# Performance work log

Measured on AMD Instinct MI355X. Metric: run time of the kernel, lower is better.

Reference implementation:

```python
import jax, jax.numpy as jnp
import numpy as np
import math

K = 8
MOMENTUM = 0.999


def _gelu(x):
    c = math.sqrt(2.0 / math.pi)
    return 0.5 * x * (1.0 + jnp.tanh(c * (x + 0.044715 * x ** 3)))


def _normalize(v, eps=1e-12):
    n = jnp.linalg.norm(v, axis=-1, keepdims=True)
    return v / jnp.maximum(n, eps)


def setup_inputs() -> dict:
    key = jax.random.key(0)
    k1, k2 = jax.random.split(key)
    B, T, D = 4, 4096, 2048
    x = jax.random.normal(k1, (B, T, D), dtype=jnp.float32)
    prototypes = _normalize(jax.random.normal(k2, (K, D), dtype=jnp.float32))
    log_tau = jnp.asarray(math.log(2.0), dtype=jnp.float32)
    log_blend = jnp.asarray(math.log(0.3 / 0.7), dtype=jnp.float32)
    return {"x": x, "prototypes": prototypes, "log_tau": log_tau, "log_blend": log_blend}


def reference(x, prototypes, log_tau, log_blend):
    tau = jnp.exp(log_tau)
    alpha = jax.nn.sigmoid(log_blend)
    B, T, D = x.shape
    x_flat = jax.lax.stop_gradient(x.reshape(-1, D))  # [N, D], detached

    P_norm = _normalize(prototypes)                  # [K, D]
    xn = _normalize(x_flat, eps=1e-8)                # [N, D]

    sims = jnp.clip(xn @ P_norm.T, -1.0, 1.0)        # [N, K]
    assignments = jnp.argmax(sims, axis=-1)          # [N]

    # masked per-cluster mean via segment-sum (vectorized over K)
    sums = jax.ops.segment_sum(x_flat, assignments, num_segments=K)       # [K, D]
    counts = jax.ops.segment_sum(jnp.ones((x_flat.shape[0],), x.dtype),
                                 assignments, num_segments=K)             # [K]
    has = (counts > 0)[:, None]
    centroids = jnp.where(has, sums / jnp.maximum(counts, 1.0)[:, None], prototypes)
    new_P = _normalize(centroids)

    P2 = MOMENTUM * prototypes + (1.0 - MOMENTUM) * new_P
    P2n = _normalize(P2, eps=1e-8)

    sims2 = jnp.clip(xn @ P2n.T, -1.0, 1.0)          # [N, K]
    dists = jnp.clip(1.0 - jnp.max(sims2, axis=-1), 0.0, 2.0)
    novelty = (1.0 - jnp.exp(-tau * dists)).reshape(B, T)

    scale = jnp.clip(1.0 - alpha + alpha * novelty[..., None], 0.1, 10.0)
    return _gelu(x * scale)
```

## Files before the change

kernel.cpp:

```cpp
#include <hip/hip_runtime.h>

#define N_TOK 16384
#define DDIM  2048
#define KC    8
#define CH1   32
#define TBA   4
#define TBF   4

typedef float nfloat4 __attribute__((ext_vector_type(4)));

__device__ __forceinline__ void nt_store4(const float4& v, float* p){
  nfloat4 nv; nv.x = v.x; nv.y = v.y; nv.z = v.z; nv.w = v.w;
  __builtin_nontemporal_store(nv, (nfloat4*)p);
}
__device__ __forceinline__ float4 nt_load4(const float* p){
  nfloat4 nv = __builtin_nontemporal_load((const nfloat4*)p);
  return make_float4(nv.x, nv.y, nv.z, nv.w);
}

__device__ __forceinline__ float wave_sum(float v){
  #pragma unroll
  for (int off = 32; off > 0; off >>= 1)
    v += __shfl_xor(v, off, 64);
  return v;
}

__device__ __forceinline__ float butterfly8(float v[8], int t){
  {
    const bool h = (t & 1);
    #pragma unroll
    for (int j = 0; j < 4; ++j){
      float s    = h ? v[j]   : v[j+4];
      float keep = h ? v[j+4] : v[j];
      v[j] = keep + __shfl_xor(s, 1, 64);
    }
  }
  {
    const bool h = (t & 2);
    #pragma unroll
    for (int j = 0; j < 2; ++j){
      float s    = h ? v[j]   : v[j+2];
      float keep = h ? v[j+2] : v[j];
      v[j] = keep + __shfl_xor(s, 2, 64);
    }
  }
  {
    const bool h = (t & 4);
    float s    = h ? v[0] : v[1];
    float keep = h ? v[1] : v[0];
    v[0] = keep + __shfl_xor(s, 4, 64);
  }
  v[0] += __shfl_xor(v[0], 8, 64);
  v[0] += __shfl_xor(v[0], 16, 64);
  v[0] += __shfl_xor(v[0], 32, 64);
  return v[0];
}

__device__ __forceinline__ float gelu_tanh(float v){
  const float c = 0.7978845608028654f;
  float tt = c * v * (1.0f + 0.044715f * v * v);
  float e  = __expf(2.0f * tt);
  float th = 1.0f - 2.0f / (e + 1.0f);
  return 0.5f * v * (1.0f + th);
}

__global__ __launch_bounds__(256, 2)
void k_assign(const float* __restrict__ x, const float* __restrict__ proto,
              float* __restrict__ psums, float* __restrict__ pcnts, int ntok)
{
  const int t = threadIdx.x;
  const int wave = t >> 6, lane = t & 63;
  const int d0 = 4*t, d1 = DDIM/2 + 4*t;
  const int kidx = ((lane&1)<<2) | (lane&2) | ((lane>>2)&1);

  __shared__ float rednorm[4*KC];
  __shared__ float red[TBA][4][KC];
  __shared__ float sInv[KC];
  __shared__ float sCnt[KC];
  __shared__ int   sAsg[TBA];

  float4 P0[KC], P1[KC];
  float4 acc0[KC], acc1[KC];
  #pragma unroll
  for (int k = 0; k < KC; ++k){
    P0[k] = *(const float4*)(proto + k*DDIM + d0);
    P1[k] = *(const float4*)(proto + k*DDIM + d1);
    acc0[k] = make_float4(0.f,0.f,0.f,0.f);
    acc1[k] = make_float4(0.f,0.f,0.f,0.f);
  }
  if (t < KC) sCnt[t] = 0.f;

  #pragma unroll
  for (int k = 0; k < KC; ++k){
    float ss = P0[k].x*P0[k].x + P0[k].y*P0[k].y + P0[k].z*P0[k].z + P0[k].w*P0[k].w
             + P1[k].x*P1[k].x + P1[k].y*P1[k].y + P1[k].z*P1[k].z + P1[k].w*P1[k].w;
    ss = wave_sum(ss);
    if (lane == 0) rednorm[wave*KC + k] = ss;
  }
  __syncthreads();
  if (t < KC){
    float ss = rednorm[t] + rednorm[KC + t] + rednorm[2*KC + t] + rednorm[3*KC + t];
    sInv[t] = 1.0f / fmaxf(sqrtf(ss), 1e-12f);
  }
  __syncthreads();

  const int stride = gridDim.x * TBA;
  float4 X0[TBA], X1[TBA], N0[TBA], N1[TBA];
  int tok0 = blockIdx.x * TBA;
  #pragma unroll
  for (int i = 0; i < TBA; ++i){
    int tk = tok0 + i;
    X0[i] = make_float4(0,0,0,0); X1[i] = make_float4(0,0,0,0);
    if (tk < ntok){
      X0[i] = *(const float4*)(x + (size_t)tk*DDIM + d0);
      X1[i] = *(const float4*)(x + (size_t)tk*DDIM + d1);
    }
  }

  for (; tok0 < ntok; tok0 += stride){
    const int ntok0 = tok0 + stride;
    #pragma unroll
    for (int i = 0; i < TBA; ++i){
      int tk = ntok0 + i;
      N0[i] = make_float4(0,0,0,0); N1[i] = make_float4(0,0,0,0);
      if (tk < ntok){
        N0[i] = *(const float4*)(x + (size_t)tk*DDIM + d0);
        N1[i] = *(const float4*)(x + (size_t)tk*DDIM + d1);
      }
    }
    #pragma unroll
    for (int i = 0; i < TBA; ++i){
      float v[KC];
      #pragma unroll
      for (int k = 0; k < KC; ++k){
        v[k] = X0[i].x*P0[k].x + X0[i].y*P0[k].y + X0[i].z*P0[k].z + X0[i].w*P0[k].w
             + X1[i].x*P1[k].x + X1[i].y*P1[k].y + X1[i].z*P1[k].z + X1[i].w*P1[k].w;
      }
      float r = butterfly8(v, t);
      if (lane < 8) red[i][wave][kidx] = r;
    }
    __syncthreads();
    if (t < TBA && tok0 + t < ntok){
      int best = 0; float bv = -3.4e38f;
      #pragma unroll
      for (int k = 0; k < KC; ++k){
        float val = (red[t][0][k] + red[t][1][k] + red[t][2][k] + red[t][3][k]) * sInv[k];
        if (val > bv){ bv = val; best = k; }
      }
      sAsg[t] = best;
      atomicAdd(&sCnt[best], 1.0f);
    }
    __syncthreads();
    #pragma unroll
    for (int i = 0; i < TBA; ++i){
      if (tok0 + i < ntok){
        const int a = sAsg[i];
        #pragma unroll
        for (int k = 0; k < KC; ++k){
          if (a == k){
            acc0[k].x += X0[i].x; acc0[k].y += X0[i].y; acc0[k].z += X0[i].z; acc0[k].w += X0[i].w;
            acc1[k].x += X1[i].x; acc1[k].y += X1[i].y; acc1[k].z += X1[i].z; acc1[k].w += X1[i].w;
          }
        }
      }
    }
    #pragma unroll
    for (int i = 0; i < TBA; ++i){ X0[i] = N0[i]; X1[i] = N1[i]; }
  }
  __syncthreads();
  float* dst = psums + (size_t)blockIdx.x * (KC*DDIM);
  #pragma unroll
  for (int k = 0; k < KC; ++k){
    nt_store4(acc0[k], dst + k*DDIM + d0);
    nt_store4(acc1[k], dst + k*DDIM + d1);
  }
  if (t < KC) pcnts[blockIdx.x*KC + t] = sCnt[t];
}

__global__ __launch_bounds__(256)
void k_reduce1(const float* __restrict__ psums, const float* __restrict__ pcnts,
               float* __restrict__ stage2, float* __restrict__ cnt2, int nb, int cs)
{
  const int ch = blockIdx.x >> 4;
  const int g  = blockIdx.x & 15;
  const int col = g*1024 + threadIdx.x*4;
  const int b0 = ch*cs;

  float4 acc = make_float4(0.f,0.f,0.f,0.f);
  #pragma unroll 4
  for (int i = 0; i < cs; ++i){
    int b = b0 + i;
    if (b < nb){
      float4 v = nt_load4(psums + (size_t)b*(KC*DDIM) + col);
      acc.x += v.x; acc.y += v.y; acc.z += v.z; acc.w += v.w;
    }
  }
  *(float4*)(stage2 + (size_t)ch*(KC*DDIM) + col) = acc;

  if (g == 0 && threadIdx.x < KC){
    float c = 0.f;
    for (int i = 0; i < cs; ++i){
      int b = b0 + i;
      if (b < nb) c += pcnts[b*KC + threadIdx.x];
    }
    cnt2[ch*KC + threadIdx.x] = c;
  }
}

__global__ __launch_bounds__(256)
void k_reduce2(const float* __restrict__ stage2, const float* __restrict__ cnt2,
               const float* __restrict__ proto, float* __restrict__ centroid)
{
  __shared__ float cnt[KC];
  if (threadIdx.x < KC){
    float c = 0.f;
    #pragma unroll
    for (int ch = 0; ch < CH1; ++ch) c += cnt2[ch*KC + threadIdx.x];
    cnt[threadIdx.x] = c;
  }
  __syncthreads();
  const int col = blockIdx.x*1024 + threadIdx.x*4;
  float4 s = make_float4(0.f,0.f,0.f,0.f);
  #pragma unroll
  for (int ch = 0; ch < CH1; ++ch){
    float4 v = *(const float4*)(stage2 + (size_t)ch*(KC*DDIM) + col);
    s.x += v.x; s.y += v.y; s.z += v.z; s.w += v.w;
  }
  const int k = col >> 11;
  const float c = cnt[k];
  float4 o;
  if (c > 0.f){
    float inv = 1.0f / fmaxf(c, 1.f);
    o.x = s.x*inv; o.y = s.y*inv; o.z = s.z*inv; o.w = s.w*inv;
  } else {
    o = *(const float4*)(proto + col);
  }
  *(float4*)(centroid + col) = o;
}

__global__ void k_pupdate(const float* __restrict__ centroid, const float* __restrict__ proto,
                          float* __restrict__ p2n)
{
  const int t = threadIdx.x;
  const int w = t >> 6, lane = t & 63;
  float4 c[8], pr[8];
  float ss = 0.f;
  #pragma unroll
  for (int j = 0; j < 8; ++j){
    const int d = (j*64 + lane)*4;
    c[j]  = *(const float4*)(centroid + w*DDIM + d);
    pr[j] = *(const float4*)(proto    + w*DDIM + d);
    ss += c[j].x*c[j].x + c[j].y*c[j].y + c[j].z*c[j].z + c[j].w*c[j].w;
  }
  ss = wave_sum(ss);
  const float invc = 1.0f / fmaxf(sqrtf(ss), 1e-12f);
  const float m = 0.999f, om = 1.0f - 0.999f;
  float4 p2[8];
  float ss2 = 0.f;
  #pragma unroll
  for (int j = 0; j < 8; ++j){
    p2[j].x = m*pr[j].x + om*c[j].x*invc;
    p2[j].y = m*pr[j].y + om*c[j].y*invc;
    p2[j].z = m*pr[j].z + om*c[j].z*invc;
    p2[j].w = m*pr[j].w + om*c[j].w*invc;
    ss2 += p2[j].x*p2[j].x + p2[j].y*p2[j].y + p2[j].z*p2[j].z + p2[j].w*p2[j].w;
  }
  ss2 = wave_sum(ss2);
  const float inv2 = 1.0f / fmaxf(sqrtf(ss2), 1e-8f);
  #pragma unroll
  for (int j = 0; j < 8; ++j){
    const int d = (j*64 + lane)*4;
    float4 o;
    o.x = p2[j].x*inv2; o.y = p2[j].y*inv2; o.z = p2[j].z*inv2; o.w = p2[j].w*inv2;
    *(float4*)(p2n + w*DDIM + d) = o;
  }
}

__global__ __launch_bounds__(256, 2)
void k_final(const float* __restrict__ x, const float* __restrict__ p2n,
             const float* __restrict__ plog_tau, const float* __restrict__ plog_blend,
             float* __restrict__ out, int ntok)
{
  const int t = threadIdx.x;
  const int wave = t >> 6, lane = t & 63;
  const int d0 = 4*t, d1 = DDIM/2 + 4*t;
  const int kidx = ((lane&1)<<2) | (lane&2) | ((lane>>2)&1);

  __shared__ float red[TBF][4][KC];
  __shared__ float redss[TBF][4];
  __shared__ float sScale[TBF];

  float4 P0[KC], P1[KC];
  #pragma unroll
  for (int k = 0; k < KC; ++k){
    P0[k] = *(const float4*)(p2n + k*DDIM + d0);
    P1[k] = *(const float4*)(p2n + k*DDIM + d1);
  }
  const float tau   = __expf(plog_tau[0]);
  const float alpha = 1.0f / (1.0f + __expf(-plog_blend[0]));

  const int stride = gridDim.x * TBF;
  float4 X0[TBF], X1[TBF], N0[TBF], N1[TBF];
  int tok0 = blockIdx.x * TBF;
  #pragma unroll
  for (int i = 0; i < TBF; ++i){
    int tk = tok0 + i;
    X0[i] = make_float4(0,0,0,0); X1[i] = make_float4(0,0,0,0);
    if (tk < ntok){
      X0[i] = *(const float4*)(x + (size_t)tk*DDIM + d0);
      X1[i] = *(const float4*)(x + (size_t)tk*DDIM + d1);
    }
  }

  for (; tok0 < ntok; tok0 += stride){
    const int ntok0 = tok0 + stride;
    #pragma unroll
    for (int i = 0; i < TBF; ++i){
      int tk = ntok0 + i;
      N0[i] = make_float4(0,0,0,0); N1[i] = make_float4(0,0,0,0);
      if (tk < ntok){
        N0[i] = *(const float4*)(x + (size_t)tk*DDIM + d0);
        N1[i] = *(const float4*)(x + (size_t)tk*DDIM + d1);
      }
    }
    #pragma unroll
    for (int i = 0; i < TBF; ++i){
      float v[KC];
      #pragma unroll
      for (int k = 0; k < KC; ++k){
        v[k] = X0[i].x*P0[k].x + X0[i].y*P0[k].y + X0[i].z*P0[k].z + X0[i].w*P0[k].w
             + X1[i].x*P1[k].x + X1[i].y*P1[k].y + X1[i].z*P1[k].z + X1[i].w*P1[k].w;
      }
      float r = butterfly8(v, t);
      if (lane < 8) red[i][wave][kidx] = r;
      float ss = X0[i].x*X0[i].x + X0[i].y*X0[i].y + X0[i].z*X0[i].z + X0[i].w*X0[i].w
               + X1[i].x*X1[i].x + X1[i].y*X1[i].y + X1[i].z*X1[i].z + X1[i].w*X1[i].w;
      ss = wave_sum(ss);
      if (lane == 0) redss[i][wave] = ss;
    }
    __syncthreads();
    if (t < TBF && tok0 + t < ntok){
      float fss = redss[t][0] + redss[t][1] + redss[t][2] + redss[t][3];
      float inv = 1.0f / fmaxf(sqrtf(fss), 1e-8f);
      float mx = -3.4e38f;
      #pragma unroll
      for (int k = 0; k < KC; ++k){
        float val = red[t][0][k] + red[t][1][k] + red[t][2][k] + red[t][3][k];
        mx = fmaxf(mx, val);
      }
      float s    = fminf(fmaxf(mx * inv, -1.0f), 1.0f);
      float dist = fminf(fmaxf(1.0f - s, 0.0f), 2.0f);
      float nov  = 1.0f - __expf(-tau * dist);
      float sc   = 1.0f - alpha + alpha * nov;
      sScale[t]  = fminf(fmaxf(sc, 0.1f), 10.0f);
    }
    __syncthreads();
    #pragma unroll
    for (int i = 0; i < TBF; ++i){
      int tk = tok0 + i;
      if (tk < ntok){
        const float sc = sScale[i];
        float* o = out + (size_t)tk*DDIM;
        float4 o0, o1;
        o0.x = gelu_tanh(X0[i].x*sc); o0.y = gelu_tanh(X0[i].y*sc);
        o0.z = gelu_tanh(X0[i].z*sc); o0.w = gelu_tanh(X0[i].w*sc);
        o1.x = gelu_tanh(X1[i].x*sc); o1.y = gelu_tanh(X1[i].y*sc);
        o1.z = gelu_tanh(X1[i].z*sc); o1.w = gelu_tanh(X1[i].w*sc);
        nt_store4(o0, o + d0);
        nt_store4(o1, o + d1);
      }
    }
    #pragma unroll
    for (int i = 0; i < TBF; ++i){ X0[i] = N0[i]; X1[i] = N1[i]; }
  }
}

extern "C" void kernel_launch(void* const* d_in, const int* in_sizes, int n_in,
                              void* d_out, int out_size, void* d_ws, size_t ws_size,
                              hipStream_t stream)
{
  const float* x          = (const float*)d_in[0];
  const float* proto      = (const float*)d_in[1];
  const float* log_tau    = (const float*)d_in[2];
  const float* log_blend  = (const float*)d_in[3];
  float* out = (float*)d_out;
  float* ws  = (float*)d_ws;

  const int ntok = in_sizes[0] / DDIM;

  float* centroid = ws;
  float* p2n      = ws + 16384;
  float* pcnts    = ws + 32768;
  float* cnt2     = ws + 36864;
  float* stage2   = ws + 37120;
  float* psums    = ws + 37120 + CH1*KC*DDIM;

  long cap = (long)(ws_size / 4) - (37120 + CH1*KC*DDIM);
  int nb = (int)(cap / (KC * DDIM));
  if (nb > 512) nb = 512;
  if (nb < 1)  nb = 1;
  const int cs = (nb + CH1 - 1) / CH1;

  k_assign <<<nb,      256, 0, stream>>>(x, proto, psums, pcnts, ntok);
  k_reduce1<<<CH1*16,  256, 0, stream>>>(psums, pcnts, stage2, cnt2, nb, cs);
  k_reduce2<<<16,      256, 0, stream>>>(stage2, cnt2, proto, centroid);
  k_pupdate<<<1,       512, 0, stream>>>(centroid, proto, p2n);
  k_final  <<<512,     256, 0, stream>>>(x, p2n, log_tau, log_blend, out, ntok);
}
```

Baseline: 308.0 us.

## Fuse pipeline into one cooperative kernel with grid syncs and bf16 partial sums

```diff
diff --git a/kernel.cpp b/kernel.cpp
--- a/kernel.cpp
+++ b/kernel.cpp
@@ -1,21 +1,31 @@
 #include <hip/hip_runtime.h>
-
-#define N_TOK 16384
+#include <hip/hip_cooperative_groups.h>
+
+namespace cg = cooperative_groups;
+
 #define DDIM  2048
 #define KC    8
 #define CH1   32
 #define TBA   4
 #define TBF   4
+#define GRID  512
 
 typedef float nfloat4 __attribute__((ext_vector_type(4)));
+typedef unsigned short ushortv8 __attribute__((ext_vector_type(8)));
+typedef unsigned short ushortv4 __attribute__((ext_vector_type(4)));
 
 __device__ __forceinline__ void nt_store4(const float4& v, float* p){
   nfloat4 nv; nv.x = v.x; nv.y = v.y; nv.z = v.z; nv.w = v.w;
   __builtin_nontemporal_store(nv, (nfloat4*)p);
 }
-__device__ __forceinline__ float4 nt_load4(const float* p){
-  nfloat4 nv = __builtin_nontemporal_load((const nfloat4*)p);
-  return make_float4(nv.x, nv.y, nv.z, nv.w);
+
+__device__ __forceinline__ unsigned short f2bf(float f){
+  unsigned u = __float_as_uint(f);
+  u += 0x7fffu + ((u >> 16) & 1u);
+  return (unsigned short)(u >> 16);
+}
+__device__ __forceinline__ float bf2f(unsigned short h){
+  return __uint_as_float(((unsigned)h) << 16);
 }
 
 __device__ __forceinline__ float wave_sum(float v){
@@ -64,9 +74,9 @@
   return 0.5f * v * (1.0f + th);
 }
 
-__global__ __launch_bounds__(256, 2)
-void k_assign(const float* __restrict__ x, const float* __restrict__ proto,
-              float* __restrict__ psums, float* __restrict__ pcnts, int ntok)
+__device__ __forceinline__ void phase_assign(const float* __restrict__ x,
+    const float* __restrict__ proto, unsigned short* __restrict__ psums,
+    float* __restrict__ pcnts, int ntok, int bid, int gsz)
 {
   const int t = threadIdx.x;
   const int wave = t >> 6, lane = t & 63;
@@ -74,13 +84,12 @@
   const int kidx = ((lane&1)<<2) | (lane&2) | ((lane>>2)&1);
 
   __shared__ float rednorm[4*KC];
-  __shared__ float red[TBA][4][KC];
-  __shared__ float sInv[KC];
+  __shared__ float redA[TBA][4][KC];
+  __shared__ float sInvA[KC];
   __shared__ float sCnt[KC];
   __shared__ int   sAsg[TBA];
 
-  float4 P0[KC], P1[KC];
-  float4 acc0[KC], acc1[KC];
+  float4 P0[KC], P1[KC], acc0[KC], acc1[KC];
   #pragma unroll
   for (int k = 0; k < KC; ++k){
     P0[k] = *(const float4*)(proto + k*DDIM + d0);
@@ -100,13 +109,13 @@
   __syncthreads();
   if (t < KC){
     float ss = rednorm[t] + rednorm[KC + t] + rednorm[2*KC + t] + rednorm[3*KC + t];
-    sInv[t] = 1.0f / fmaxf(sqrtf(ss), 1e-12f);
+    sInvA[t] = 1.0f / fmaxf(sqrtf(ss), 1e-12f);
   }
   __syncthreads();
 
-  const int stride = gridDim.x * TBA;
+  const int stride = gsz * TBA;
   float4 X0[TBA], X1[TBA], N0[TBA], N1[TBA];
-  int tok0 = blockIdx.x * TBA;
+  int tok0 = bid * TBA;
   #pragma unroll
   for (int i = 0; i < TBA; ++i){
     int tk = tok0 + i;
@@ -137,14 +146,14 @@
              + X1[i].x*P1[k].x + X1[i].y*P1[k].y + X1[i].z*P1[k].z + X1[i].w*P1[k].w;
       }
       float r = butterfly8(v, t);
-      if (lane < 8) red[i][wave][kidx] = r;
+      if (lane < 8) redA[i][wave][kidx] = r;
     }
     __syncthreads();
     if (t < TBA && tok0 + t < ntok){
       int best = 0; float bv = -3.4e38f;
       #pragma unroll
       for (int k = 0; k < KC; ++k){
-        float val = (red[t][0][k] + red[t][1][k] + red[t][2][k] + red[t][3][k]) * sInv[k];
+        float val = (redA[t][0][k] + redA[t][1][k] + redA[t][2][k] + redA[t][3][k]) * sInvA[k];
         if (val > bv){ bv = val; best = k; }
       }
       sAsg[t] = best;
@@ -154,7 +163,7 @@
     #pragma unroll
     for (int i = 0; i < TBA; ++i){
       if (tok0 + i < ntok){
-        const int a = sAsg[i];
+        const int a = __builtin_amdgcn_readfirstlane(sAsg[i]);
         #pragma unroll
         for (int k = 0; k < KC; ++k){
           if (a == k){
@@ -168,140 +177,138 @@
     for (int i = 0; i < TBA; ++i){ X0[i] = N0[i]; X1[i] = N1[i]; }
   }
   __syncthreads();
-  float* dst = psums + (size_t)blockIdx.x * (KC*DDIM);
+
+  unsigned short* dst = psums + (size_t)bid * (KC*DDIM);
   #pragma unroll
   for (int k = 0; k < KC; ++k){
-    nt_store4(acc0[k], dst + k*DDIM + d0);
-    nt_store4(acc1[k], dst + k*DDIM + d1);
-  }
-  if (t < KC) pcnts[blockIdx.x*KC + t] = sCnt[t];
-}
-
-__global__ __launch_bounds__(256)
-void k_reduce1(const float* __restrict__ psums, const float* __restrict__ pcnts,
-               float* __restrict__ stage2, float* __restrict__ cnt2, int nb, int cs)
-{
-  const int ch = blockIdx.x >> 4;
-  const int g  = blockIdx.x & 15;
-  const int col = g*1024 + threadIdx.x*4;
-  const int b0 = ch*cs;
-
-  float4 acc = make_float4(0.f,0.f,0.f,0.f);
-  #pragma unroll 4
-  for (int i = 0; i < cs; ++i){
-    int b = b0 + i;
-    if (b < nb){
-      float4 v = nt_load4(psums + (size_t)b*(KC*DDIM) + col);
-      acc.x += v.x; acc.y += v.y; acc.z += v.z; acc.w += v.w;
-    }
-  }
-  *(float4*)(stage2 + (size_t)ch*(KC*DDIM) + col) = acc;
-
-  if (g == 0 && threadIdx.x < KC){
-    float c = 0.f;
+    ushortv8 o;
+    o[0] = f2bf(acc0[k].x); o[1] = f2bf(acc0[k].y); o[2] = f2bf(acc0[k].z); o[3] = f2bf(acc0[k].w);
+    o[4] = f2bf(acc1[k].x); o[5] = f2bf(acc1[k].y); o[6] = f2bf(acc1[k].z); o[7] = f2bf(acc1[k].w);
+    *(ushortv8*)(dst + k*DDIM + t*8) = o;
+  }
+  if (t < KC) pcnts[bid*KC + t] = sCnt[t];
+}
+
+__device__ __forceinline__ void phase_reduce1(const unsigned short* __restrict__ psums,
+    const float* __restrict__ pcnts, float* __restrict__ stage2, float* __restrict__ cnt2,
+    int nb, int bid, int gsz)
+{
+  const int cs = (nb + CH1 - 1) / CH1;
+  for (int job = bid; job < CH1*16; job += gsz){
+    const int ch = job >> 4;
+    const int gq = job & 15;
+    const int col = gq*1024 + threadIdx.x*4;
+    const int b0 = ch*cs;
+    float4 acc = make_float4(0.f,0.f,0.f,0.f);
+    #pragma unroll 4
     for (int i = 0; i < cs; ++i){
       int b = b0 + i;
-      if (b < nb) c += pcnts[b*KC + threadIdx.x];
-    }
-    cnt2[ch*KC + threadIdx.x] = c;
-  }
-}
-
-__global__ __launch_bounds__(256)
-void k_reduce2(const float* __restrict__ stage2, const float* __restrict__ cnt2,
-               const float* __restrict__ proto, float* __restrict__ centroid)
-{
-  __shared__ float cnt[KC];
-  if (threadIdx.x < KC){
+      if (b < nb){
+        ushortv4 v = *(const ushortv4*)(psums + (size_t)b*(KC*DDIM) + col);
+        acc.x += bf2f(v[0]); acc.y += bf2f(v[1]); acc.z += bf2f(v[2]); acc.w += bf2f(v[3]);
+      }
+    }
+    *(float4*)(stage2 + (size_t)ch*(KC*DDIM) + col) = acc;
+
+    if (gq == 0 && threadIdx.x < KC){
+      float c = 0.f;
+      for (int i = 0; i < cs; ++i){
+        int b = b0 + i;
+        if (b < nb) c += pcnts[b*KC + threadIdx.x];
+      }
+      cnt2[ch*KC + threadIdx.x] = c;
+    }
+  }
+}
+
+__device__ __forceinline__ void phase_mid(const float* __restrict__ stage2,
+    const float* __restrict__ cnt2, const float* __restrict__ proto,
+    float* __restrict__ p2n, int bid)
+{
+  __shared__ float sR1[4], sR2[4];
+  if (bid < KC){
+    const int k = bid, t = threadIdx.x;
+    const int wave = t >> 6, lane = t & 63;
+
     float c = 0.f;
     #pragma unroll
-    for (int ch = 0; ch < CH1; ++ch) c += cnt2[ch*KC + threadIdx.x];
-    cnt[threadIdx.x] = c;
-  }
-  __syncthreads();
-  const int col = blockIdx.x*1024 + threadIdx.x*4;
-  float4 s = make_float4(0.f,0.f,0.f,0.f);
-  #pragma unroll
-  for (int ch = 0; ch < CH1; ++ch){
-    float4 v = *(const float4*)(stage2 + (size_t)ch*(KC*DDIM) + col);
-    s.x += v.x; s.y += v.y; s.z += v.z; s.w += v.w;
-  }
-  const int k = col >> 11;
-  const float c = cnt[k];
-  float4 o;
-  if (c > 0.f){
-    float inv = 1.0f / fmaxf(c, 1.f);
-    o.x = s.x*inv; o.y = s.y*inv; o.z = s.z*inv; o.w = s.w*inv;
-  } else {
-    o = *(const float4*)(proto + col);
-  }
-  *(float4*)(centroid + col) = o;
-}
-
-__global__ void k_pupdate(const float* __restrict__ centroid, const float* __restrict__ proto,
-                          float* __restrict__ p2n)
-{
-  const int t = threadIdx.x;
-  const int w = t >> 6, lane = t & 63;
-  float4 c[8], pr[8];
-  float ss = 0.f;
-  #pragma unroll
-  for (int j = 0; j < 8; ++j){
-    const int d = (j*64 + lane)*4;
-    c[j]  = *(const float4*)(centroid + w*DDIM + d);
-    pr[j] = *(const float4*)(proto    + w*DDIM + d);
-    ss += c[j].x*c[j].x + c[j].y*c[j].y + c[j].z*c[j].z + c[j].w*c[j].w;
-  }
-  ss = wave_sum(ss);
-  const float invc = 1.0f / fmaxf(sqrtf(ss), 1e-12f);
-  const float m = 0.999f, om = 1.0f - 0.999f;
-  float4 p2[8];
-  float ss2 = 0.f;
-  #pragma unroll
-  for (int j = 0; j < 8; ++j){
-    p2[j].x = m*pr[j].x + om*c[j].x*invc;
-    p2[j].y = m*pr[j].y + om*c[j].y*invc;
-    p2[j].z = m*pr[j].z + om*c[j].z*invc;
-    p2[j].w = m*pr[j].w + om*c[j].w*invc;
-    ss2 += p2[j].x*p2[j].x + p2[j].y*p2[j].y + p2[j].z*p2[j].z + p2[j].w*p2[j].w;
-  }
-  ss2 = wave_sum(ss2);
-  const float inv2 = 1.0f / fmaxf(sqrtf(ss2), 1e-8f);
-  #pragma unroll
-  for (int j = 0; j < 8; ++j){
-    const int d = (j*64 + lane)*4;
-    float4 o;
-    o.x = p2[j].x*inv2; o.y = p2[j].y*inv2; o.z = p2[j].z*inv2; o.w = p2[j].w*inv2;
-    *(float4*)(p2n + w*DDIM + d) = o;
-  }
-}
-
-__global__ __launch_bounds__(256, 2)
-void k_final(const float* __restrict__ x, const float* __restrict__ p2n,
-             const float* __restrict__ plog_tau, const float* __restrict__ plog_blend,
-             float* __restrict__ out, int ntok)
+    for (int ch = 0; ch < CH1; ++ch) c += cnt2[ch*KC + k];
+
+    float4 s0 = make_float4(0.f,0.f,0.f,0.f), s1 = make_float4(0.f,0.f,0.f,0.f);
+    #pragma unroll
+    for (int ch = 0; ch < CH1; ++ch){
+      const float* p = stage2 + (size_t)ch*(KC*DDIM) + k*DDIM + t*8;
+      float4 a = *(const float4*)p;
+      float4 b = *(const float4*)(p + 4);
+      s0.x += a.x; s0.y += a.y; s0.z += a.z; s0.w += a.w;
+      s1.x += b.x; s1.y += b.y; s1.z += b.z; s1.w += b.w;
+    }
+    float4 pr0 = *(const float4*)(proto + k*DDIM + 4*t);
+    float4 pr1 = *(const float4*)(proto + k*DDIM + DDIM/2 + 4*t);
+
+    float4 c0, c1;
+    if (c > 0.f){
+      float inv = 1.0f / fmaxf(c, 1.f);
+      c0.x = s0.x*inv; c0.y = s0.y*inv; c0.z = s0.z*inv; c0.w = s0.w*inv;
+      c1.x = s1.x*inv; c1.y = s1.y*inv; c1.z = s1.z*inv; c1.w = s1.w*inv;
+    } else { c0 = pr0; c1 = pr1; }
+
+    float ss = c0.x*c0.x + c0.y*c0.y + c0.z*c0.z + c0.w*c0.w
+             + c1.x*c1.x + c1.y*c1.y + c1.z*c1.z + c1.w*c1.w;
+    ss = wave_sum(ss);
+    if (lane == 0) sR1[wave] = ss;
+    __syncthreads();
+    ss = sR1[0] + sR1[1] + sR1[2] + sR1[3];
+    const float invc = 1.0f / fmaxf(sqrtf(ss), 1e-12f);
+
+    const float m = 0.999f, om = 1.0f - 0.999f;
+    float4 p20, p21;
+    p20.x = m*pr0.x + om*c0.x*invc; p20.y = m*pr0.y + om*c0.y*invc;
+    p20.z = m*pr0.z + om*c0.z*invc; p20.w = m*pr0.w + om*c0.w*invc;
+    p21.x = m*pr1.x + om*c1.x*invc; p21.y = m*pr1.y + om*c1.y*invc;
+    p21.z = m*pr1.z + om*c1.z*invc; p21.w = m*pr1.w + om*c1.w*invc;
+
+    float ss2 = p20.x*p20.x + p20.y*p20.y + p20.z*p20.z + p20.w*p20.w
+              + p21.x*p21.x + p21.y*p21.y + p21.z*p21.z + p21.w*p21.w;
+    ss2 = wave_sum(ss2);
+    if (lane == 0) sR2[wave] = ss2;
+    __syncthreads();
+    ss2 = sR2[0] + sR2[1] + sR2[2] + sR2[3];
+    const float inv2 = 1.0f / fmaxf(sqrtf(ss2), 1e-8f);
+
+    float4 o0, o1;
+    o0.x = p20.x*inv2; o0.y = p20.y*inv2; o0.z = p20.z*inv2; o0.w = p20.w*inv2;
+    o1.x = p21.x*inv2; o1.y = p21.y*inv2; o1.z = p21.z*inv2; o1.w = p21.w*inv2;
+    *(float4*)(p2n + k*DDIM + t*8)     = o0;
+    *(float4*)(p2n + k*DDIM + t*8 + 4) = o1;
+  }
+}
+
+__device__ __forceinline__ void phase_final(const float* __restrict__ x,
+    const float* __restrict__ p2n, const float* __restrict__ plt,
+    const float* __restrict__ plb, float* __restrict__ out, int ntok, int bid, int gsz)
 {
   const int t = threadIdx.x;
   const int wave = t >> 6, lane = t & 63;
   const int d0 = 4*t, d1 = DDIM/2 + 4*t;
   const int kidx = ((lane&1)<<2) | (lane&2) | ((lane>>2)&1);
 
-  __shared__ float red[TBF][4][KC];
+  __shared__ float redF[TBF][4][KC];
   __shared__ float redss[TBF][4];
   __shared__ float sScale[TBF];
 
   float4 P0[KC], P1[KC];
   #pragma unroll
   for (int k = 0; k < KC; ++k){
-    P0[k] = *(const float4*)(p2n + k*DDIM + d0);
-    P1[k] = *(const float4*)(p2n + k*DDIM + d1);
-  }
-  const float tau   = __expf(plog_tau[0]);
-  const float alpha = 1.0f / (1.0f + __expf(-plog_blend[0]));
-
-  const int stride = gridDim.x * TBF;
+    P0[k] = *(const float4*)(p2n + k*DDIM + t*8);
+    P1[k] = *(const float4*)(p2n + k*DDIM + t*8 + 4);
+  }
+  const float tau   = __expf(plt[0]);
+  const float alpha = 1.0f / (1.0f + __expf(-plb[0]));
+
+  const int stride = gsz * TBF;
   float4 X0[TBF], X1[TBF], N0[TBF], N1[TBF];
-  int tok0 = blockIdx.x * TBF;
+  int tok0 = bid * TBF;
   #pragma unroll
   for (int i = 0; i < TBF; ++i){
     int tk = tok0 + i;
@@ -332,7 +339,7 @@
              + X1[i].x*P1[k].x + X1[i].y*P1[k].y + X1[i].z*P1[k].z + X1[i].w*P1[k].w;
       }
       float r = butterfly8(v, t);
-      if (lane < 8) red[i][wave][kidx] = r;
+      if (lane < 8) redF[i][wave][kidx] = r;
       float ss = X0[i].x*X0[i].x + X0[i].y*X0[i].y + X0[i].z*X0[i].z + X0[i].w*X0[i].w
                + X1[i].x*X1[i].x + X1[i].y*X1[i].y + X1[i].z*X1[i].z + X1[i].w*X1[i].w;
       ss = wave_sum(ss);
@@ -345,7 +352,7 @@
       float mx = -3.4e38f;
       #pragma unroll
       for (int k = 0; k < KC; ++k){
-        float val = red[t][0][k] + red[t][1][k] + red[t][2][k] + red[t][3][k];
+        float val = redF[t][0][k] + redF[t][1][k] + redF[t][2][k] + redF[t][3][k];
         mx = fmaxf(mx, val);
       }
       float s    = fminf(fmaxf(mx * inv, -1.0f), 1.0f);
@@ -375,6 +382,51 @@
   }
 }
 
+__global__ __launch_bounds__(256, 2)
+void k_fused(const float* __restrict__ x, const float* __restrict__ proto,
+             const float* __restrict__ plt, const float* __restrict__ plb,
+             float* __restrict__ out, float* __restrict__ ws, int ntok)
+{
+  float* p2n    = ws;
+  float* pcnts  = ws + 16384;
+  float* cnt2   = ws + 20480;
+  float* stage2 = ws + 20736;
+  unsigned short* psums = (unsigned short*)(ws + 20736 + CH1*KC*DDIM);
+
+  const int bid = blockIdx.x;
+  const int gsz = gridDim.x;
+  cg::grid_group grid = cg::this_grid();
+
+  phase_assign(x, proto, psums, pcnts, ntok, bid, gsz);
+  grid.sync();
+  phase_reduce1(psums, pcnts, stage2, cnt2, gsz, bid, gsz);
+  grid.sync();
+  phase_mid(stage2, cnt2, proto, p2n, bid);
+  grid.sync();
+  phase_final(x, p2n, plt, plb, out, ntok, bid, gsz);
+}
+
+__global__ __launch_bounds__(256, 2)
+void k_s1(const float* __restrict__ x, const float* __restrict__ proto,
+          unsigned short* __restrict__ psums, float* __restrict__ pcnts, int ntok)
+{ phase_assign(x, proto, psums, pcnts, ntok, blockIdx.x, gridDim.x); }
+
+__global__ __launch_bounds__(256)
+void k_s2(const unsigned short* __restrict__ psums, const float* __restrict__ pcnts,
+          float* __restrict__ stage2, float* __restrict__ cnt2, int nb)
+{ phase_reduce1(psums, pcnts, stage2, cnt2, nb, blockIdx.x, gridDim.x); }
+
+__global__ __launch_bounds__(256)
+void k_s3(const float* __restrict__ stage2, const float* __restrict__ cnt2,
+          const float* __restrict__ proto, float* __restrict__ p2n)
+{ phase_mid(stage2, cnt2, proto, p2n, blockIdx.x); }
+
+__global__ __launch_bounds__(256, 2)
+void k_s4(const float* __restrict__ x, const float* __restrict__ p2n,
+          const float* __restrict__ plt, const float* __restrict__ plb,
+          float* __restrict__ out, int ntok)
+{ phase_final(x, p2n, plt, plb, out, ntok, blockIdx.x, gridDim.x); }
+
 extern "C" void kernel_launch(void* const* d_in, const int* in_sizes, int n_in,
                               void* d_out, int out_size, void* d_ws, size_t ws_size,
                               hipStream_t stream)
@@ -388,22 +440,25 @@
 
   const int ntok = in_sizes[0] / DDIM;
 
-  float* centroid = ws;
-  float* p2n      = ws + 16384;
-  float* pcnts    = ws + 32768;
-  float* cnt2     = ws + 36864;
-  float* stage2   = ws + 37120;
-  float* psums    = ws + 37120 + CH1*KC*DDIM;
-
-  long cap = (long)(ws_size / 4) - (37120 + CH1*KC*DDIM);
-  int nb = (int)(cap / (KC * DDIM));
-  if (nb > 512) nb = 512;
-  if (nb < 1)  nb = 1;
-  const int cs = (nb + CH1 - 1) / CH1;
-
-  k_assign <<<nb,      256, 0, stream>>>(x, proto, psums, pcnts, ntok);
-  k_reduce1<<<CH1*16,  256, 0, stream>>>(psums, pcnts, stage2, cnt2, nb, cs);
-  k_reduce2<<<16,      256, 0, stream>>>(stage2, cnt2, proto, centroid);
-  k_pupdate<<<1,       512, 0, stream>>>(centroid, proto, p2n);
-  k_final  <<<512,     256, 0, stream>>>(x, p2n, log_tau, log_blend, out, ntok);
-}
+  float* p2n    = ws;
+  float* pcnts  = ws + 16384;
+  float* cnt2   = ws + 20480;
+  float* stage2 = ws + 20736;
+  unsigned short* psums = (unsigned short*)(ws + 20736 + CH1*KC*DDIM);
+
+  const float* xa = x; const float* pa = proto;
+  const float* lta = log_tau; const float* lba = log_blend;
+  float* oa = out; float* wa = ws; int na = ntok;
+  void* args[7] = { (void*)&xa, (void*)&pa, (void*)&lta, (void*)&lba,
+                    (void*)&oa, (void*)&wa, (void*)&na };
+
+  hipError_t err = hipLaunchCooperativeKernel((const void*)k_fused,
+                                              dim3(GRID), dim3(256), args, 0, stream);
+  if (err != hipSuccess){
+    (void)hipGetLastError();
+    k_s1<<<GRID,   256, 0, stream>>>(x, proto, psums, pcnts, ntok);
+    k_s2<<<CH1*16, 256, 0, stream>>>(psums, pcnts, stage2, cnt2, GRID);
+    k_s3<<<KC,     256, 0, stream>>>(stage2, cnt2, proto, p2n);
+    k_s4<<<GRID,   256, 0, stream>>>(x, p2n, log_tau, log_blend, out, ntok);
+  }
+}
```

After: 475.4 us. 1.54x slower.
